# Performance work log

Hardware: AMD Instinct MI355X
Metric: run time of the kernel (lower is better)

The kernel has to match this reference:

```python
import jax, jax.numpy as jnp
import numpy as np

NUM_FEATURES = 2048
NUM_SAMPLES = 16384
SOURCE_CLASSES = 1024
TEMP = 0.05
MOMENTUM = 0.2
BATCH = 256
SPECIAL_LABEL = 5554  # hard-coded remap in the original forward (is_source=True path)


def setup_inputs() -> dict:
    key = jax.random.key(0)
    k1, k2, k3 = jax.random.split(key, 3)
    inputs = jax.random.normal(k1, (BATCH, NUM_FEATURES), dtype=jnp.float32)
    inputs = inputs / jnp.linalg.norm(inputs, axis=1, keepdims=True)  # re-ID features are L2-normalized
    targets = jax.random.randint(k2, (BATCH,), 0, NUM_SAMPLES)  # 1-based labels; 0 -> invalid after -1 shift
    features = jax.random.normal(k3, (NUM_SAMPLES, NUM_FEATURES), dtype=jnp.float32)
    features = features / jnp.linalg.norm(features, axis=1, keepdims=True)
    return {"inputs": inputs, "targets": targets, "features": features}


def reference(inputs, targets, features):
    ignore = SOURCE_CLASSES - 1
    t = targets - 1
    t = jnp.where(t == SPECIAL_LABEL, ignore, t)  # remap special label to ignore_index class
    # torch drops rows with t < 0 before the mm and cross_entropy ignores ignore_index;
    # rows are independent under row-wise softmax, so masking is equivalent to filtering.
    valid = (t >= 0) & (t != ignore)
    logits = (inputs @ features.T) / TEMP  # [B, NUM_SAMPLES]
    logp = jax.nn.log_softmax(logits, axis=-1)
    tc = jnp.clip(t, 0, NUM_SAMPLES - 1)
    nll = -jnp.take_along_axis(logp, tc[:, None], axis=1)[:, 0]  # [B]
    n_valid = jnp.sum(valid)
    loss = jnp.sum(jnp.where(valid, nll, 0.0)) / jnp.maximum(n_valid, 1).astype(nll.dtype)
    return loss
```

## Files before the change

kernel.cpp:

```cpp
#include <hip/hip_runtime.h>
#include <hip/hip_bf16.h>

typedef __attribute__((ext_vector_type(4))) float f32x4;
typedef __attribute__((ext_vector_type(8))) short s16x8;

#define M_DIM 256
#define N_DIM 16384
#define K_DIM 2048
#define BM 128
#define BN 128
#define BK 32
#define LDS_PITCH 40
#define NKT (K_DIM / BK)
#define TEMP_INV 20.0f
#define SPECIAL 5554
#define IGNORE_IDX 1023

__device__ __forceinline__ short f2bf(float x) {
  __hip_bfloat16 h = __float2bfloat16(x);
  return __builtin_bit_cast(short, h);
}

__device__ __forceinline__ void cvt_store(short* dst, const float4& f0, const float4& f1) {
  s16x8 h;
  h[0] = f2bf(f0.x); h[1] = f2bf(f0.y); h[2] = f2bf(f0.z); h[3] = f2bf(f0.w);
  h[4] = f2bf(f1.x); h[5] = f2bf(f1.y); h[6] = f2bf(f1.z); h[7] = f2bf(f1.w);
  *reinterpret_cast<s16x8*>(dst) = h;
}

__global__ __launch_bounds__(512, 1) void gemm_fused(
    const float* __restrict__ A, const float* __restrict__ B,
    const int* __restrict__ targets,
    float* __restrict__ partial,
    float* __restrict__ targ) {
  __shared__ __align__(16) short As[2][BM * LDS_PITCH];
  __shared__ __align__(16) short Bs[2][BN * LDS_PITCH];
  __shared__ int tcs[BM];
  __shared__ float rsum[BM][4];

  int bid = blockIdx.x;
  int lbid = (bid & 7) * 32 + (bid >> 3);
  int bm = lbid & 1;
  int bn = lbid >> 1;

  int tid = threadIdx.x;
  int wave = tid >> 6;
  int lane = tid & 63;
  int wm = wave >> 2;
  int wn = wave & 3;

  if (tid < BM) {
    int tt = targets[bm * BM + tid] - 1;
    if (tt == SPECIAL) tt = IGNORE_IDX;
    int tc = tt < 0 ? 0 : (tt > N_DIM - 1 ? N_DIM - 1 : tt);
    tcs[tid] = tc;
  }

  int srow = tid >> 2;
  int squad = tid & 3;
  const float* aG = A + (size_t)(bm * BM + srow) * K_DIM + squad * 8;
  const float* bG = B + (size_t)(bn * BN + srow) * K_DIM + squad * 8;
  int swoff = srow * LDS_PITCH + squad * 8;

  f32x4 acc[4][2];
#pragma unroll
  for (int mi = 0; mi < 4; ++mi)
#pragma unroll
    for (int ni = 0; ni < 2; ++ni)
      acc[mi][ni] = f32x4{0.f, 0.f, 0.f, 0.f};

  float4 rA[2][2], rB[2][2];

  rA[0][0] = *(const float4*)(aG);      rA[0][1] = *(const float4*)(aG + 4);
  rB[0][0] = *(const float4*)(bG);      rB[0][1] = *(const float4*)(bG + 4);
  cvt_store(&As[0][swoff], rA[0][0], rA[0][1]);
  cvt_store(&Bs[0][swoff], rB[0][0], rB[0][1]);
  rA[1][0] = *(const float4*)(aG + BK); rA[1][1] = *(const float4*)(aG + BK + 4);
  rB[1][0] = *(const float4*)(bG + BK); rB[1][1] = *(const float4*)(bG + BK + 4);
  __syncthreads();

  int arow0 = (wm * 64 + (lane & 15)) * LDS_PITCH + (lane >> 4) * 8;
  int brow0 = (wn * 32 + (lane & 15)) * LDS_PITCH + (lane >> 4) * 8;

  for (int ktb = 0; ktb < NKT; ktb += 2) {
#pragma unroll
    for (int u = 0; u < 2; ++u) {
      int kt = ktb + u;
      const short* asb = &As[u][0];
      const short* bsb = &Bs[u][0];
      s16x8 af[4], bfr[2];
#pragma unroll
      for (int mi = 0; mi < 4; ++mi)
        af[mi] = *reinterpret_cast<const s16x8*>(asb + arow0 + mi * 16 * LDS_PITCH);
#pragma unroll
      for (int ni = 0; ni < 2; ++ni)
        bfr[ni] = *reinterpret_cast<const s16x8*>(bsb + brow0 + ni * 16 * LDS_PITCH);
#pragma unroll
      for (int mi = 0; mi < 4; ++mi)
#pragma unroll
        for (int ni = 0; ni < 2; ++ni)
          acc[mi][ni] = __builtin_amdgcn_mfma_f32_16x16x32_bf16(
              af[mi], bfr[ni], acc[mi][ni], 0, 0, 0);

      if (kt + 1 < NKT) {
        cvt_store(&As[u ^ 1][swoff], rA[u ^ 1][0], rA[u ^ 1][1]);
        cvt_store(&Bs[u ^ 1][swoff], rB[u ^ 1][0], rB[u ^ 1][1]);
        if (kt + 2 < NKT) {
          const float* ap = aG + (size_t)(kt + 2) * BK;
          const float* bp = bG + (size_t)(kt + 2) * BK;
          rA[u][0] = *(const float4*)ap;  rA[u][1] = *(const float4*)(ap + 4);
          rB[u][0] = *(const float4*)bp;  rB[u][1] = *(const float4*)(bp + 4);
        }
        __syncthreads();
      }
    }
  }

  int g = lane >> 4;
  int cl = lane & 15;
  int gcol_base = bn * BN + wn * 32 + cl;
#pragma unroll
  for (int mi = 0; mi < 4; ++mi) {
#pragma unroll
    for (int r = 0; r < 4; ++r) {
      int rl = wm * 64 + mi * 16 + g * 4 + r;
      int tc = tcs[rl];
      float s = 0.f;
#pragma unroll
      for (int ni = 0; ni < 2; ++ni) {
        float logit = acc[mi][ni][r] * TEMP_INV;
        if (gcol_base + ni * 16 == tc) targ[bm * BM + rl] = logit;
        s += __expf(logit);
      }
#pragma unroll
      for (int m = 1; m < 16; m <<= 1) s += __shfl_xor(s, m, 64);
      if (cl == 0) rsum[rl][wn] = s;
    }
  }
  __syncthreads();
  if (tid < BM) {
    float s = rsum[tid][0] + rsum[tid][1] + rsum[tid][2] + rsum[tid][3];
    partial[(size_t)bn * M_DIM + bm * BM + tid] = s;
  }
}

__global__ __launch_bounds__(256) void finalize(
    const float* __restrict__ partial, const float* __restrict__ targ,
    const int* __restrict__ targets, float* __restrict__ out) {
  int r = threadIdx.x;
  float s = 0.f;
  for (int j = 0; j < 128; ++j) s += partial[(size_t)j * M_DIM + r];
  int t = targets[r] - 1;
  if (t == SPECIAL) t = IGNORE_IDX;
  bool valid = (t >= 0) && (t != IGNORE_IDX);
  float nl = logf(s) - targ[r];
  float sv = valid ? nl : 0.0f;
  float cv = valid ? 1.0f : 0.0f;
#pragma unroll
  for (int m = 1; m < 64; m <<= 1) {
    sv += __shfl_xor(sv, m, 64);
    cv += __shfl_xor(cv, m, 64);
  }
  __shared__ float ss[4], cc[4];
  int wid = r >> 6, lane = r & 63;
  if (lane == 0) { ss[wid] = sv; cc[wid] = cv; }
  __syncthreads();
  if (r == 0) {
    float S = ss[0] + ss[1] + ss[2] + ss[3];
    float C = cc[0] + cc[1] + cc[2] + cc[3];
    out[0] = S / fmaxf(C, 1.0f);
  }
}

extern "C" void kernel_launch(void* const* d_in, const int* in_sizes, int n_in,
                              void* d_out, int out_size, void* d_ws, size_t ws_size,
                              hipStream_t stream) {
  const float* inputs   = (const float*)d_in[0];
  const int*   targets  = (const int*)d_in[1];
  const float* features = (const float*)d_in[2];
  float* out = (float*)d_out;

  float* partial = (float*)d_ws;
  float* targ    = partial + (size_t)128 * M_DIM;

  gemm_fused<<<dim3(256), dim3(512), 0, stream>>>(inputs, features, targets, partial, targ);
  finalize<<<dim3(1), dim3(256), 0, stream>>>(partial, targ, targets, out);
}
```

Baseline: 43.04 us.

## Pre-convert A to swizzled bf16 and stream B directly into registers

Adds a pre-pass kernel that converts the inputs matrix to bf16 in a swizzled, tile-ordered layout. The GEMM then loads A tiles into LDS with global_load_lds and feeds B straight from global memory into MFMA fragments, with no LDS staging for B. Tiles change from 128x128 to 64x256, so each block covers a 256-column strip and the finalize kernel sums 64 partials instead of 128. This is meant to cut per-block fp32 conversion of A, most LDS traffic and barriers, and the redundant reads of the feature matrix. In exchange it adds an extra kernel launch, and B fragments are now read per wave from global memory without LDS reuse.

New measurement: 78.19 us. 1.82x slower.

```diff
diff --git a/kernel.cpp b/kernel.cpp
--- a/kernel.cpp
+++ b/kernel.cpp
@@ -7,11 +7,12 @@
 #define M_DIM 256
 #define N_DIM 16384
 #define K_DIM 2048
-#define BM 128
-#define BN 128
+#define BM 64
+#define BN 256
 #define BK 32
-#define LDS_PITCH 40
-#define NKT (K_DIM / BK)
+#define NKT 64
+#define TPG 8
+#define NG 8
 #define TEMP_INV 20.0f
 #define SPECIAL 5554
 #define IGNORE_IDX 1023
@@ -21,127 +22,153 @@
   return __builtin_bit_cast(short, h);
 }
 
-__device__ __forceinline__ void cvt_store(short* dst, const float4& f0, const float4& f1) {
+__device__ __forceinline__ void gload_lds16(const void* g, void* l) {
+  __builtin_amdgcn_global_load_lds((const __attribute__((address_space(1))) void*)g,
+                                   (__attribute__((address_space(3))) void*)l, 16, 0, 0);
+}
+
+__global__ __launch_bounds__(256) void convA(const float* __restrict__ A,
+                                             short* __restrict__ Abf) {
+  int fid = blockIdx.x * 256 + threadIdx.x;
+  int bm = fid >> 14;
+  int kt = (fid >> 8) & 63;
+  int q = fid & 255;
+  int r = q >> 2;
+  int cp = q & 3;
+  int c = cp ^ ((r >> 1) & 3);
+  const float* src = A + (size_t)(bm * BM + r) * K_DIM + kt * BK + c * 8;
+  float4 lo = *(const float4*)src;
+  float4 hi = *(const float4*)(src + 4);
   s16x8 h;
-  h[0] = f2bf(f0.x); h[1] = f2bf(f0.y); h[2] = f2bf(f0.z); h[3] = f2bf(f0.w);
-  h[4] = f2bf(f1.x); h[5] = f2bf(f1.y); h[6] = f2bf(f1.z); h[7] = f2bf(f1.w);
-  *reinterpret_cast<s16x8*>(dst) = h;
+  h[0] = f2bf(lo.x); h[1] = f2bf(lo.y); h[2] = f2bf(lo.z); h[3] = f2bf(lo.w);
+  h[4] = f2bf(hi.x); h[5] = f2bf(hi.y); h[6] = f2bf(hi.z); h[7] = f2bf(hi.w);
+  *reinterpret_cast<s16x8*>(Abf + (size_t)fid * 8) = h;
 }
 
 __global__ __launch_bounds__(512, 1) void gemm_fused(
-    const float* __restrict__ A, const float* __restrict__ B,
+    const short* __restrict__ Abf, const float* __restrict__ B,
     const int* __restrict__ targets,
     float* __restrict__ partial,
     float* __restrict__ targ) {
-  __shared__ __align__(16) short As[2][BM * LDS_PITCH];
-  __shared__ __align__(16) short Bs[2][BN * LDS_PITCH];
+  __shared__ __align__(16) short Abuf[2][TPG * BM * BK];
   __shared__ int tcs[BM];
-  __shared__ float rsum[BM][4];
+  __shared__ float rsum[BM][8];
 
   int bid = blockIdx.x;
   int lbid = (bid & 7) * 32 + (bid >> 3);
-  int bm = lbid & 1;
-  int bn = lbid >> 1;
+  int bm = lbid & 3;
+  int bn = lbid >> 2;
 
   int tid = threadIdx.x;
   int wave = tid >> 6;
   int lane = tid & 63;
-  int wm = wave >> 2;
-  int wn = wave & 3;
+  int rl = lane & 15;
+  int kq = lane >> 4;
 
   if (tid < BM) {
     int tt = targets[bm * BM + tid] - 1;
     if (tt == SPECIAL) tt = IGNORE_IDX;
-    int tc = tt < 0 ? 0 : (tt > N_DIM - 1 ? N_DIM - 1 : tt);
-    tcs[tid] = tc;
-  }
-
-  int srow = tid >> 2;
-  int squad = tid & 3;
-  const float* aG = A + (size_t)(bm * BM + srow) * K_DIM + squad * 8;
-  const float* bG = B + (size_t)(bn * BN + srow) * K_DIM + squad * 8;
-  int swoff = srow * LDS_PITCH + squad * 8;
+    tcs[tid] = tt < 0 ? 0 : (tt > N_DIM - 1 ? N_DIM - 1 : tt);
+  }
+
+  const float* bptr0 = B + (size_t)(bn * BN + wave * 32 + rl) * K_DIM + kq * 8;
+
+  int bmBase = bm * (NKT * 256);
+
+  int soff = rl * 32 + ((kq ^ ((rl >> 1) & 3)) << 3);
 
   f32x4 acc[4][2];
 #pragma unroll
-  for (int mi = 0; mi < 4; ++mi)
-#pragma unroll
-    for (int ni = 0; ni < 2; ++ni)
-      acc[mi][ni] = f32x4{0.f, 0.f, 0.f, 0.f};
-
-  float4 rA[2][2], rB[2][2];
-
-  rA[0][0] = *(const float4*)(aG);      rA[0][1] = *(const float4*)(aG + 4);
-  rB[0][0] = *(const float4*)(bG);      rB[0][1] = *(const float4*)(bG + 4);
-  cvt_store(&As[0][swoff], rA[0][0], rA[0][1]);
-  cvt_store(&Bs[0][swoff], rB[0][0], rB[0][1]);
-  rA[1][0] = *(const float4*)(aG + BK); rA[1][1] = *(const float4*)(aG + BK + 4);
-  rB[1][0] = *(const float4*)(bG + BK); rB[1][1] = *(const float4*)(bG + BK + 4);
+  for (int m = 0; m < 4; ++m)
+#pragma unroll
+    for (int ni = 0; ni < 2; ++ni) acc[m][ni] = f32x4{0.f, 0.f, 0.f, 0.f};
+
+  float4 Bpre[2][2][2];
+
+#define LOADB(par, kt)                                                        \
+  {                                                                           \
+    const float* _p = bptr0 + (size_t)(kt) * BK;                              \
+    Bpre[par][0][0] = *(const float4*)_p;                                     \
+    Bpre[par][0][1] = *(const float4*)(_p + 4);                               \
+    Bpre[par][1][0] = *(const float4*)(_p + 16 * K_DIM);                      \
+    Bpre[par][1][1] = *(const float4*)(_p + 16 * K_DIM + 4);                  \
+  }
+
+#define STAGE(g, bufidx)                                                      \
+  {                                                                           \
+    int _base = bmBase + (g) * (TPG * 256);                                   \
+    char* _lb = (char*)&Abuf[bufidx][0];                                      \
+    _Pragma("unroll") for (int _j = 0; _j < 4; ++_j) {                        \
+      int _ci = _j * 512 + tid;                                               \
+      gload_lds16(Abf + ((size_t)(_base + _ci) << 3), _lb + _ci * 16);        \
+    }                                                                         \
+  }
+
+  STAGE(0, 0);
+  LOADB(0, 0);
+  LOADB(1, 1);
   __syncthreads();
 
-  int arow0 = (wm * 64 + (lane & 15)) * LDS_PITCH + (lane >> 4) * 8;
-  int brow0 = (wn * 32 + (lane & 15)) * LDS_PITCH + (lane >> 4) * 8;
-
-  for (int ktb = 0; ktb < NKT; ktb += 2) {
-#pragma unroll
-    for (int u = 0; u < 2; ++u) {
-      int kt = ktb + u;
-      const short* asb = &As[u][0];
-      const short* bsb = &Bs[u][0];
-      s16x8 af[4], bfr[2];
-#pragma unroll
-      for (int mi = 0; mi < 4; ++mi)
-        af[mi] = *reinterpret_cast<const s16x8*>(asb + arow0 + mi * 16 * LDS_PITCH);
-#pragma unroll
-      for (int ni = 0; ni < 2; ++ni)
-        bfr[ni] = *reinterpret_cast<const s16x8*>(bsb + brow0 + ni * 16 * LDS_PITCH);
-#pragma unroll
-      for (int mi = 0; mi < 4; ++mi)
+  for (int g = 0; g < NG; ++g) {
+    if (g + 1 < NG) STAGE(g + 1, (g + 1) & 1);
+    const short* ab = &Abuf[g & 1][0];
+#pragma unroll
+    for (int t = 0; t < TPG; ++t) {
+      s16x8 bf[2];
+#pragma unroll
+      for (int ni = 0; ni < 2; ++ni) {
+        float4 lo = Bpre[t & 1][ni][0], hi = Bpre[t & 1][ni][1];
+        s16x8 h;
+        h[0] = f2bf(lo.x); h[1] = f2bf(lo.y); h[2] = f2bf(lo.z); h[3] = f2bf(lo.w);
+        h[4] = f2bf(hi.x); h[5] = f2bf(hi.y); h[6] = f2bf(hi.z); h[7] = f2bf(hi.w);
+        bf[ni] = h;
+      }
+      int ktB = g * TPG + t + 2;
+      if (ktB < NKT) LOADB(t & 1, ktB);
+
+      s16x8 af[4];
+#pragma unroll
+      for (int m = 0; m < 4; ++m)
+        af[m] = *reinterpret_cast<const s16x8*>(ab + t * 2048 + m * 512 + soff);
+
+#pragma unroll
+      for (int m = 0; m < 4; ++m)
 #pragma unroll
         for (int ni = 0; ni < 2; ++ni)
-          acc[mi][ni] = __builtin_amdgcn_mfma_f32_16x16x32_bf16(
-              af[mi], bfr[ni], acc[mi][ni], 0, 0, 0);
-
-      if (kt + 1 < NKT) {
-        cvt_store(&As[u ^ 1][swoff], rA[u ^ 1][0], rA[u ^ 1][1]);
-        cvt_store(&Bs[u ^ 1][swoff], rB[u ^ 1][0], rB[u ^ 1][1]);
-        if (kt + 2 < NKT) {
-          const float* ap = aG + (size_t)(kt + 2) * BK;
-          const float* bp = bG + (size_t)(kt + 2) * BK;
-          rA[u][0] = *(const float4*)ap;  rA[u][1] = *(const float4*)(ap + 4);
-          rB[u][0] = *(const float4*)bp;  rB[u][1] = *(const float4*)(bp + 4);
-        }
-        __syncthreads();
-      }
+          acc[m][ni] = __builtin_amdgcn_mfma_f32_16x16x32_bf16(
+              af[m], bf[ni], acc[m][ni], 0, 0, 0);
     }
-  }
-
-  int g = lane >> 4;
-  int cl = lane & 15;
-  int gcol_base = bn * BN + wn * 32 + cl;
-#pragma unroll
-  for (int mi = 0; mi < 4; ++mi) {
+    __syncthreads();
+  }
+
+  int colbase = bn * BN + wave * 32 + rl;
+#pragma unroll
+  for (int m = 0; m < 4; ++m) {
 #pragma unroll
     for (int r = 0; r < 4; ++r) {
-      int rl = wm * 64 + mi * 16 + g * 4 + r;
-      int tc = tcs[rl];
+      int rloc = m * 16 + kq * 4 + r;
+      int tc = tcs[rloc];
       float s = 0.f;
 #pragma unroll
       for (int ni = 0; ni < 2; ++ni) {
-        float logit = acc[mi][ni][r] * TEMP_INV;
-        if (gcol_base + ni * 16 == tc) targ[bm * BM + rl] = logit;
+        float logit = acc[m][ni][r] * TEMP_INV;
+        if (colbase + ni * 16 == tc) targ[bm * BM + rloc] = logit;
         s += __expf(logit);
       }
 #pragma unroll
-      for (int m = 1; m < 16; m <<= 1) s += __shfl_xor(s, m, 64);
-      if (cl == 0) rsum[rl][wn] = s;
+      for (int msk = 1; msk < 16; msk <<= 1) s += __shfl_xor(s, msk, 64);
+      if (rl == 0) rsum[rloc][wave] = s;
     }
   }
   __syncthreads();
   if (tid < BM) {
-    float s = rsum[tid][0] + rsum[tid][1] + rsum[tid][2] + rsum[tid][3];
+    float s = 0.f;
+#pragma unroll
+    for (int w = 0; w < 8; ++w) s += rsum[tid][w];
     partial[(size_t)bn * M_DIM + bm * BM + tid] = s;
   }
+#undef LOADB
+#undef STAGE
 }
 
 __global__ __launch_bounds__(256) void finalize(
@@ -149,7 +176,7 @@
     const int* __restrict__ targets, float* __restrict__ out) {
   int r = threadIdx.x;
   float s = 0.f;
-  for (int j = 0; j < 128; ++j) s += partial[(size_t)j * M_DIM + r];
+  for (int j = 0; j < 64; ++j) s += partial[(size_t)j * M_DIM + r];
   int t = targets[r] - 1;
   if (t == SPECIAL) t = IGNORE_IDX;
   bool valid = (t >= 0) && (t != IGNORE_IDX);
@@ -180,9 +207,11 @@
   const float* features = (const float*)d_in[2];
   float* out = (float*)d_out;
 
-  float* partial = (float*)d_ws;
-  float* targ    = partial + (size_t)128 * M_DIM;
-
-  gemm_fused<<<dim3(256), dim3(512), 0, stream>>>(inputs, features, targets, partial, targ);
+  short* Abf     = (short*)d_ws;
+  float* partial = (float*)((char*)d_ws + (1 << 20));
+  float* targ    = partial + 64 * M_DIM;
+
+  convA<<<dim3(256), dim3(256), 0, stream>>>(inputs, Abf);
+  gemm_fused<<<dim3(256), dim3(512), 0, stream>>>(Abf, features, targets, partial, targ);
   finalize<<<dim3(1), dim3(256), 0, stream>>>(partial, targ, targets, out);
 }
```
